# Kernel optimization log

Hardware: AMD Instinct MI355X
Metric: run time of the kernel (lower is better)

The kernel has to match this reference:

```python
import jax, jax.numpy as jnp
import numpy as np

# Dims: B=4, C_in=256, H=W=64 -> L=4096, token_dim D=256, state_dim N=512, K=4
B_, C_IN, H_, W_ = 4, 256, 64, 64
D, N, K = 256, 512, 4


def setup_inputs() -> dict:
    key = jax.random.key(0)
    ks = jax.random.split(key, 16)
    g = lambda k, shape, sc=0.02: (jax.random.normal(k, shape, jnp.float32) * sc)
    return {
        'feat_map': jax.random.normal(ks[0], (B_, C_IN, H_, W_), jnp.float32),
        'hf_map':   jax.random.normal(ks[1], (B_, C_IN, H_, W_), jnp.float32),
        # 1x1 conv proj_f / proj_hf: weight (out=D, in=C_IN), bias (D,)
        'Wf':  g(ks[2], (D, C_IN)), 'bf':  jnp.zeros((D,), jnp.float32),
        'Whf': g(ks[3], (D, C_IN)), 'bhf': jnp.zeros((D,), jnp.float32),
        # alpha_head: Linear(D, D//2) -> GELU -> Linear(D//2, K)
        'Wa1': g(ks[4], (D // 2, D)), 'ba1': jnp.zeros((D // 2,), jnp.float32),
        'Wa2': g(ks[5], (K, D // 2)), 'ba2': jnp.zeros((K,), jnp.float32),
        # SelectiveSSM base tuples: diagonal decay logits A (K,N), input maps B (K,N,D), output maps C (K,D,N)
        'A_base': g(ks[6], (K, N), 1.0),
        'B_base': g(ks[7], (K, N, D), 0.02),
        'C_base': g(ks[8], (K, D, N), 0.02),
        # out_proj 1x1 conv: (C_IN, D)
        'Wout': g(ks[9], (C_IN, D)), 'bout': jnp.zeros((C_IN,), jnp.float32),
    }


def _stage(feat_map, hf_map, Wf, bf, Whf, bhf, Wa1, ba1, Wa2, ba2,
           A_base, B_base, C_base, Wout, bout):
    B, C, H, W = feat_map.shape
    L = H * W
    # 1x1 conv token projections -> (B, L, D)
    t_f = jnp.einsum('bchw,dc->bdhw', feat_map, Wf) + bf[None, :, None, None]
    t_hf = jnp.einsum('bchw,dc->bdhw', hf_map, Whf) + bhf[None, :, None, None]
    x = t_f.reshape(B, -1, L).transpose(0, 2, 1)        # (B, L, D)
    t_hf_seq = t_hf.reshape(B, -1, L).transpose(0, 2, 1)  # (B, L, D)
    # gating MLP -> per-token mixture weights over K base SSMs
    hmid = jax.nn.gelu(t_hf_seq @ Wa1.T + ba1, approximate=False)
    alpha = jax.nn.softmax(hmid @ Wa2.T + ba2, axis=-1)  # (B, L, K)
    # selective SSM: per-token mixed diagonal decay and input drive
    a = jax.nn.sigmoid(jnp.einsum('blk,kn->bln', alpha, A_base))   # (B, L, N)
    u = jnp.einsum('bld,blk,knd->bln', x, alpha, B_base)           # (B, L, N)

    def step(h, au):
        a_t, u_t = au                   # each (B, N)
        h = a_t * h + u_t
        return h, h

    h0 = jnp.zeros((B, a.shape[-1]), x.dtype)
    _, hs = jax.lax.scan(step, h0, (a.transpose(1, 0, 2), u.transpose(1, 0, 2)))
    h_seq = hs.transpose(1, 0, 2)                                   # (B, L, N)
    # mixed readout
    y = jnp.einsum('blk,bln,kdn->bld', alpha, h_seq, C_base)        # (B, L, D)
    y_map = y.transpose(0, 2, 1).reshape(B, -1, H, W)
    out = jnp.einsum('bdhw,cd->bchw', y_map, Wout) + bout[None, :, None, None]
    return out


def reference(feat_map, hf_map, Wf, bf, Whf, bhf, Wa1, ba1, Wa2, ba2,
              A_base, B_base, C_base, Wout, bout):
    return _stage(feat_map, hf_map, Wf, bf, Whf, bhf, Wa1, ba1, Wa2, ba2,
                  A_base, B_base, C_base, Wout, bout)
```

## Files before the change

kernel.cpp:

```cpp
#include <hip/hip_runtime.h>
#include <hip/hip_bf16.h>
#include <math.h>

#define B_  4
#define CIN 256
#define L_  4096
#define D_  256
#define N_  512
#define K_  4
#define DH  128
#define BL  (B_ * L_)

#define NCHUNK 128
#define CLEN   (L_ / NCHUNK)

typedef __attribute__((ext_vector_type(8))) short bfrag;
typedef __attribute__((ext_vector_type(4))) float f4;

__device__ __forceinline__ float bf2f(unsigned short u) {
  return __uint_as_float(((unsigned int)u) << 16);
}
__device__ __forceinline__ unsigned short f2bf(float f) {
  unsigned int u = __float_as_uint(f);
  return (unsigned short)((u + 0x7FFFu + ((u >> 16) & 1u)) >> 16);
}

__global__ void k_prep(const float* __restrict__ Wf, const float* __restrict__ Whf,
                       const float* __restrict__ Wa1, const float* __restrict__ Wout,
                       const float* __restrict__ Bb, const float* __restrict__ Cb,
                       const float* __restrict__ bfv, const float* __restrict__ bhfv,
                       unsigned short* __restrict__ Wfb ,
                       unsigned short* __restrict__ Wa1b,
                       unsigned short* __restrict__ Woutb,
                       unsigned short* __restrict__ Bb16,
                       unsigned short* __restrict__ Cb16,
                       float* __restrict__ biascat) {
  int i = blockIdx.x * 256 + threadIdx.x;
  if (i < 65536) { Wfb[i] = f2bf(Wf[i]); return; } i -= 65536;
  if (i < 65536) { Wfb[65536 + i] = f2bf(Whf[i]); return; } i -= 65536;
  if (i < 32768) { Wa1b[i] = f2bf(Wa1[i]); return; } i -= 32768;
  if (i < 65536) { Woutb[i] = f2bf(Wout[i]); return; } i -= 65536;
  if (i < 524288) {
    int d = i & 255, n = (i >> 8) & 511, k = i >> 17;
    Bb16[(((size_t)n << 2) | k) << 8 | d] = f2bf(Bb[i]);
    return;
  } i -= 524288;
  if (i < 524288) {
    int nn = i & 511, d = (i >> 9) & 255, k = i >> 17;
    Cb16[(((size_t)d << 2) | k) << 9 | nn] = f2bf(Cb[i]);
    return;
  } i -= 524288;
  if (i < 256) { biascat[i] = bfv[i]; return; } i -= 256;
  if (i < 256) { biascat[256 + i] = bhfv[i]; }
}

__global__ void k_transpose2(const float* __restrict__ feat, const float* __restrict__ hf,
                             unsigned short* __restrict__ featT ) {
  __shared__ float tile[32][33];
  const int z = blockIdx.z;
  const int b = z & 3, which = z >> 2;
  const float* in = which ? hf : feat;
  unsigned short* outT = featT + (size_t)which * BL * CIN;
  const int l0 = blockIdx.x * 32, c0 = blockIdx.y * 32;
  const int tx = threadIdx.x, ty = threadIdx.y;
  const float* p = in + ((size_t)b * CIN + c0 + ty) * L_ + l0 + tx;
#pragma unroll
  for (int i = 0; i < 32; i += 8) tile[ty + i][tx] = p[(size_t)i * L_];
  __syncthreads();
  unsigned short* q = outT + ((size_t)b * L_ + l0 + ty) * CIN + c0 + tx;
#pragma unroll
  for (int i = 0; i < 32; i += 8) q[(size_t)i * CIN] = f2bf(tile[tx][ty + i]);
}

__global__ void k_alpha(const unsigned short* __restrict__ hm0,
                        const unsigned short* __restrict__ hm1,
                        const float* __restrict__ ba1, const float* __restrict__ Wa2,
                        const float* __restrict__ ba2, float* __restrict__ alpha) {
  __shared__ float w2[K_ * DH];
  __shared__ float b1[DH];
  __shared__ float b2[K_];
  for (int i = threadIdx.x; i < K_ * DH; i += 256) w2[i] = Wa2[i];
  if (threadIdx.x < DH) b1[threadIdx.x] = ba1[threadIdx.x];
  if (threadIdx.x < K_) b2[threadIdx.x] = ba2[threadIdx.x];
  __syncthreads();
  const int token = blockIdx.x * 64 + (threadIdx.x >> 2);
  const int q = threadIdx.x & 3;
  float a0 = 0.f, a1 = 0.f, a2 = 0.f, a3 = 0.f;
  const size_t base = (size_t)token * DH + q * 32;
#pragma unroll
  for (int j8 = 0; j8 < 4; ++j8) {
    uint4 v0 = *(const uint4*)(hm0 + base + j8 * 8);
    uint4 v1 = *(const uint4*)(hm1 + base + j8 * 8);
    const unsigned int* pa = (const unsigned int*)&v0;
    const unsigned int* pb = (const unsigned int*)&v1;
#pragma unroll
    for (int p = 0; p < 4; ++p) {
      float h0 = bf2f((unsigned short)(pa[p] & 0xffffu)) +
                 bf2f((unsigned short)(pb[p] & 0xffffu));
      float h1 = bf2f((unsigned short)(pa[p] >> 16)) +
                 bf2f((unsigned short)(pb[p] >> 16));
      const int d = q * 32 + j8 * 8 + p * 2;
      float g0 = h0 + b1[d];
      float g1 = h1 + b1[d + 1];
      g0 = 0.5f * g0 * (1.0f + erff(g0 * 0.70710678118654752f));
      g1 = 0.5f * g1 * (1.0f + erff(g1 * 0.70710678118654752f));
      a0 += g0 * w2[0 * DH + d] + g1 * w2[0 * DH + d + 1];
      a1 += g0 * w2[1 * DH + d] + g1 * w2[1 * DH + d + 1];
      a2 += g0 * w2[2 * DH + d] + g1 * w2[2 * DH + d + 1];
      a3 += g0 * w2[3 * DH + d] + g1 * w2[3 * DH + d + 1];
    }
  }
  a0 += __shfl_xor(a0, 1); a1 += __shfl_xor(a1, 1); a2 += __shfl_xor(a2, 1); a3 += __shfl_xor(a3, 1);
  a0 += __shfl_xor(a0, 2); a1 += __shfl_xor(a1, 2); a2 += __shfl_xor(a2, 2); a3 += __shfl_xor(a3, 2);
  a0 += b2[0]; a1 += b2[1]; a2 += b2[2]; a3 += b2[3];
  float m = fmaxf(fmaxf(a0, a1), fmaxf(a2, a3));
  float e0 = expf(a0 - m), e1 = expf(a1 - m), e2 = expf(a2 - m), e3 = expf(a3 - m);
  float inv = 1.f / (e0 + e1 + e2 + e3);
  float my = (q == 0) ? e0 : (q == 1) ? e1 : (q == 2) ? e2 : e3;
  alpha[(size_t)token * 4 + q] = my * inv;
}


__global__ void k_scanA(const unsigned short* __restrict__ u, const float* __restrict__ alpha,
                        const float* __restrict__ Abase,
                        float* __restrict__ P, float* __restrict__ Hend) {
  const int n = threadIdx.x;
  const int bc = blockIdx.x;
  const int b = bc >> 7, c = bc & 127;
  const float A0 = Abase[n], A1 = Abase[N_ + n], A2 = Abase[2 * N_ + n], A3 = Abase[3 * N_ + n];
  const size_t tok0 = (size_t)b * L_ + (size_t)c * CLEN;
  float p = 1.f, h = 0.f;
  for (int l = 0; l < CLEN; ++l) {
    const size_t t = tok0 + l;
    float4 al = *(const float4*)(alpha + t * 4);
    float s = al.x * A0 + al.y * A1 + al.z * A2 + al.w * A3;
    float av = 1.f / (1.f + expf(-s));
    float uv = bf2f(u[t * N_ + n]);
    h = av * h + uv;
    p *= av;
  }
  P[(size_t)bc * N_ + n] = p;
  Hend[(size_t)bc * N_ + n] = h;
}

__global__ void k_scanB(const float* __restrict__ P, const float* __restrict__ Hend,
                        float* __restrict__ Hstart) {
  const int n = threadIdx.x;
  const int b = blockIdx.x;
  float h = 0.f;
  for (int c = 0; c < NCHUNK; ++c) {
    size_t idx = ((size_t)b * NCHUNK + c) * N_ + n;
    Hstart[idx] = h;
    h = P[idx] * h + Hend[idx];
  }
}

__global__ void k_scanC(const unsigned short* __restrict__ u, const float* __restrict__ alpha,
                        const float* __restrict__ Abase, const float* __restrict__ Hstart,
                        unsigned short* __restrict__ hbf) {
  const int n = threadIdx.x;
  const int bc = blockIdx.x;
  const int b = bc >> 7, c = bc & 127;
  const float A0 = Abase[n], A1 = Abase[N_ + n], A2 = Abase[2 * N_ + n], A3 = Abase[3 * N_ + n];
  const size_t tok0 = (size_t)b * L_ + (size_t)c * CLEN;
  float h = Hstart[(size_t)bc * N_ + n];
  for (int l = 0; l < CLEN; ++l) {
    const size_t t = tok0 + l;
    float4 al = *(const float4*)(alpha + t * 4);
    float s = al.x * A0 + al.y * A1 + al.z * A2 + al.w * A3;
    float av = 1.f / (1.f + expf(-s));
    float uv = bf2f(u[t * N_ + n]);
    h = av * h + uv;
    hbf[t * N_ + n] = f2bf(h);
  }
}

#define BM 128
#define BN 128
#define BK 32

#define GLL(src, dst)                                                                      \
  __builtin_amdgcn_global_load_lds((const __attribute__((address_space(1))) void*)(src),   \
                                   (__attribute__((address_space(3))) void*)(dst), 16, 0, 0)

#define BM2 128
#define BN2 256

template <int BIAS, int EPI>
__global__ __launch_bounds__(512, 2) void gemm_bt2(
    const unsigned short* __restrict__ A, long sA,
    const unsigned short* __restrict__ Bm, long sB,
    const float* __restrict__ bias, long bS,
    const float* __restrict__ alphaP,
    void* __restrict__ Cv, long sC,
    int M, int N, int Kd, int lda, int ldb) {
  const int zb = blockIdx.z;
  A += (size_t)zb * sA;
  Bm += (size_t)zb * sB;
  if (BIAS) bias += (size_t)zb * bS;
  const int m0 = blockIdx.x * BM2;
  const int n0 = blockIdx.y * BN2;
  __shared__ __attribute__((aligned(16))) unsigned short As[3 * BM2 * BK];
  __shared__ __attribute__((aligned(16))) unsigned short Bs[3 * BN2 * BK];
  const int t = threadIdx.x;
  const int lane = t & 63;
  const int w = t >> 6;
  const int wm = (w >> 2) * 64;
  const int wn = (w & 3) * 64;

  f4 acc[4][4];
#pragma unroll
  for (int i = 0; i < 4; ++i)
#pragma unroll
    for (int j = 0; j < 4; ++j) acc[i][j] = (f4){0.f, 0.f, 0.f, 0.f};

  const int rS = t >> 2;
  const int cS = (((t & 3) ^ ((t >> 3) & 3))) * 8;
  const unsigned short* gA = A + (size_t)(m0 + rS) * lda + cS;
  const unsigned short* gB = Bm + (size_t)(n0 + rS) * ldb + cS;
  const long rowStepB = (long)128 * ldb;
  const int r16 = lane & 15;
  const int sx = (r16 >> 1) & 3;
  const int kg = (((lane >> 4) ^ sx)) * 8;

#define STAGE2(slot, kt)                                                \
  do {                                                                  \
    const unsigned short* sA_ = gA + (size_t)(kt) * BK;                 \
    const unsigned short* sB_ = gB + (size_t)(kt) * BK;                 \
    unsigned short* dA_ = As + (slot) * (BM2 * BK) + t * 8;             \
    unsigned short* dB_ = Bs + (slot) * (BN2 * BK) + t * 8;             \
    GLL(sA_, dA_);                                                      \
    GLL(sB_, dB_);                                                      \
    GLL(sB_ + rowStepB, dB_ + BM2 * BK);                                \
  } while (0)

  const int nIter = Kd / BK;
  STAGE2(0, 0);
  STAGE2(1, 1);
  int slot = 0;
  for (int kt = 0; kt < nIter; ++kt) {
    if (kt + 1 < nIter) asm volatile("s_waitcnt vmcnt(3)" ::: "memory");
    else                asm volatile("s_waitcnt vmcnt(0)" ::: "memory");
    __builtin_amdgcn_s_barrier();
    asm volatile("" ::: "memory");
    if (kt + 2 < nIter) {
      int s2 = slot + 2; if (s2 >= 3) s2 -= 3;
      STAGE2(s2, kt + 2);
    }
    const unsigned short* Ab = As + slot * (BM2 * BK);
    const unsigned short* Bb2 = Bs + slot * (BN2 * BK);
    bfrag af[4], bfr[4];
#pragma unroll
    for (int i = 0; i < 4; ++i) {
      af[i]  = *(const bfrag*)(Ab + (wm + i * 16 + r16) * BK + kg);
      bfr[i] = *(const bfrag*)(Bb2 + (wn + i * 16 + r16) * BK + kg);
    }
    __builtin_amdgcn_s_setprio(1);
#pragma unroll
    for (int i = 0; i < 4; ++i)
#pragma unroll
      for (int j = 0; j < 4; ++j)
        acc[i][j] = __builtin_amdgcn_mfma_f32_16x16x32_bf16(af[i], bfr[j], acc[i][j], 0, 0, 0);
    __builtin_amdgcn_s_setprio(0);
    asm volatile("" ::: "memory");
    slot = (slot == 2) ? 0 : slot + 1;
  }
#undef STAGE2

  const int rowBase = m0 + wm + ((lane >> 4) << 2);
  const int colBase = n0 + wn + (lane & 15);

  if (EPI >= 2) {
    const int kq = lane & 3;
    const int NO = N >> 2;
    float av[4][4];
#pragma unroll
    for (int i = 0; i < 4; ++i)
#pragma unroll
      for (int r = 0; r < 4; ++r)
        av[i][r] = alphaP[(size_t)(rowBase + i * 16 + r) * 4 + kq];
    float* Cf = (float*)Cv + (size_t)zb * sC;
    unsigned short* Cb = (unsigned short*)Cv + (size_t)zb * sC;
#pragma unroll
    for (int i = 0; i < 4; ++i)
#pragma unroll
      for (int j = 0; j < 4; ++j) {
        const int col = colBase + j * 16;
#pragma unroll
        for (int r = 0; r < 4; ++r) {
          float p = av[i][r] * acc[i][j][r];
          p += __shfl_xor(p, 1);
          p += __shfl_xor(p, 2);
          if (kq == 0) {
            const int row = rowBase + i * 16 + r;
            if (EPI == 2) Cf[(size_t)row * NO + (col >> 2)] = p;
            else          Cb[(size_t)row * NO + (col >> 2)] = f2bf(p);
          }
        }
      }
    return;
  }

  float* Cf = (float*)Cv + (size_t)zb * sC;
  unsigned short* Cb = (unsigned short*)Cv + (size_t)zb * sC;
#pragma unroll
  for (int i = 0; i < 4; ++i) {
#pragma unroll
    for (int j = 0; j < 4; ++j) {
      const int col = colBase + j * 16;
#pragma unroll
      for (int r = 0; r < 4; ++r) {
        const int row = rowBase + i * 16 + r;
        float v = acc[i][j][r];
        if (BIAS == 1) v += bias[col];
        if (BIAS == 2) v += bias[row];
        if (EPI == 1) Cb[(size_t)row * N + col] = f2bf(v);
        else          Cf[(size_t)row * N + col] = v;
      }
    }
  }
}

template <int BIAS, int EPI >
__global__ __launch_bounds__(512, 2) void gemm_w8(
    const unsigned short* __restrict__ A, long sA,
    const unsigned short* __restrict__ Bm, long sB,
    const float* __restrict__ bias, long bS,
    void* __restrict__ Cv, long sC,
    int M, int N, int Kd, int lda, int ldb) {
  const int zb = blockIdx.z;
  A += (size_t)zb * sA;
  Bm += (size_t)zb * sB;
  if (BIAS) bias += (size_t)zb * bS;
  const int m0 = blockIdx.x * BM;
  const int n0 = blockIdx.y * BN;
  __shared__ __attribute__((aligned(16))) unsigned short As[3 * BM * BK];
  __shared__ __attribute__((aligned(16))) unsigned short Bs[3 * BN * BK];
  const int t = threadIdx.x;
  const int lane = t & 63;
  const int w = t >> 6;
  const int wm = (w >> 2) * 64;
  const int wn = (w & 3) * 32;

  f4 acc[4][2];
#pragma unroll
  for (int i = 0; i < 4; ++i)
#pragma unroll
    for (int j = 0; j < 2; ++j) acc[i][j] = (f4){0.f, 0.f, 0.f, 0.f};

  const int rS = t >> 2;
  const int cS = (((t & 3) ^ ((t >> 3) & 3))) * 8;
  const unsigned short* gA = A + (size_t)(m0 + rS) * lda + cS;
  const unsigned short* gB = Bm + (size_t)(n0 + rS) * ldb + cS;
  const int r16 = lane & 15;
  const int sx = (r16 >> 1) & 3;
  const int kg = (((lane >> 4) ^ sx)) * 8;

#define STAGEW(slot, kt)                                                \
  do {                                                                  \
    GLL(gA + (size_t)(kt) * BK, As + (slot) * (BM * BK) + t * 8);       \
    GLL(gB + (size_t)(kt) * BK, Bs + (slot) * (BN * BK) + t * 8);       \
  } while (0)

  const int nIter = Kd / BK;
  STAGEW(0, 0);
  STAGEW(1, 1);
  int slot = 0;
  for (int kt = 0; kt < nIter; ++kt) {
    if (kt + 1 < nIter) asm volatile("s_waitcnt vmcnt(2)" ::: "memory");
    else                asm volatile("s_waitcnt vmcnt(0)" ::: "memory");
    __builtin_amdgcn_s_barrier();
    asm volatile("" ::: "memory");
    if (kt + 2 < nIter) {
      int s2 = slot + 2; if (s2 >= 3) s2 -= 3;
      STAGEW(s2, kt + 2);
    }
    const unsigned short* Ab = As + slot * (BM * BK);
    const unsigned short* Bb2 = Bs + slot * (BN * BK);
    bfrag af[4], bfr[2];
#pragma unroll
    for (int i = 0; i < 4; ++i)
      af[i]  = *(const bfrag*)(Ab + (wm + i * 16 + r16) * BK + kg);
#pragma unroll
    for (int j = 0; j < 2; ++j)
      bfr[j] = *(const bfrag*)(Bb2 + (wn + j * 16 + r16) * BK + kg);
    __builtin_amdgcn_s_setprio(1);
#pragma unroll
    for (int i = 0; i < 4; ++i)
#pragma unroll
      for (int j = 0; j < 2; ++j)
        acc[i][j] = __builtin_amdgcn_mfma_f32_16x16x32_bf16(af[i], bfr[j], acc[i][j], 0, 0, 0);
    __builtin_amdgcn_s_setprio(0);
    asm volatile("" ::: "memory");
    slot = (slot == 2) ? 0 : slot + 1;
  }
#undef STAGEW

  const int rowBase = m0 + wm + ((lane >> 4) << 2);
  const int colBase = n0 + wn + (lane & 15);
  float* Cf = (float*)Cv + (size_t)zb * sC;
  unsigned short* Cb = (unsigned short*)Cv + (size_t)zb * sC;
#pragma unroll
  for (int i = 0; i < 4; ++i) {
#pragma unroll
    for (int j = 0; j < 2; ++j) {
      const int col = colBase + j * 16;
#pragma unroll
      for (int r = 0; r < 4; ++r) {
        const int row = rowBase + i * 16 + r;
        float v = acc[i][j][r];
        if (BIAS == 1) v += bias[col];
        if (BIAS == 2) v += bias[row];
        if (EPI == 1) Cb[(size_t)row * N + col] = f2bf(v);
        else          Cf[(size_t)row * N + col] = v;
      }
    }
  }
}


extern "C" void kernel_launch(void* const* d_in, const int* in_sizes, int n_in,
                              void* d_out, int out_size, void* d_ws, size_t ws_size,
                              hipStream_t stream) {
  const float* feat  = (const float*)d_in[0];
  const float* hf    = (const float*)d_in[1];
  const float* Wf    = (const float*)d_in[2];
  const float* bfv   = (const float*)d_in[3];
  const float* Whf   = (const float*)d_in[4];
  const float* bhfv  = (const float*)d_in[5];
  const float* Wa1   = (const float*)d_in[6];
  const float* ba1   = (const float*)d_in[7];
  const float* Wa2   = (const float*)d_in[8];
  const float* ba2   = (const float*)d_in[9];
  const float* Abase = (const float*)d_in[10];
  const float* Bbase = (const float*)d_in[11];
  const float* Cbase = (const float*)d_in[12];
  const float* Wout  = (const float*)d_in[13];
  const float* bout  = (const float*)d_in[14];
  float* out = (float*)d_out;

  char* ws = (char*)d_ws;
  size_t off = 0;
  auto alloc = [&](size_t bytes) { void* p = ws + off; off += bytes; return p; };

  unsigned short* Wfb    = (unsigned short*)alloc((size_t)2 * D_ * CIN * 2);
  unsigned short* Wa1b   = (unsigned short*)alloc((size_t)DH * D_ * 2);
  unsigned short* Woutb  = (unsigned short*)alloc((size_t)CIN * D_ * 2);
  unsigned short* Bb16   = (unsigned short*)alloc((size_t)K_ * N_ * D_ * 2);
  unsigned short* Cb16   = (unsigned short*)alloc((size_t)K_ * D_ * N_ * 2);
  float*          biascat= (float*)alloc((size_t)2 * D_ * 4);
  float*          alpha  = (float*)alloc((size_t)BL * K_ * 4);
  float*          Pc     = (float*)alloc((size_t)B_ * NCHUNK * N_ * 4);
  float*          He     = (float*)alloc((size_t)B_ * NCHUNK * N_ * 4);
  float*          Hs     = (float*)alloc((size_t)B_ * NCHUNK * N_ * 4);
  unsigned short* hbf    = (unsigned short*)alloc((size_t)BL * N_ * 2);
  unsigned short* x      = (unsigned short*)alloc((size_t)BL * D_ * 2);
  unsigned short* thf    = (unsigned short*)alloc((size_t)BL * D_ * 2);
  unsigned short* featT  = (unsigned short*)alloc((size_t)BL * CIN * 2);
  unsigned short* hfT    = (unsigned short*)alloc((size_t)BL * CIN * 2);
  unsigned short* u16    = (unsigned short*)alloc((size_t)BL * N_ * 2);

  unsigned short* hm0 = featT;
  unsigned short* hm1 = featT + (size_t)BL * DH;
  unsigned short* y   = thf;

  if (ws_size < off) return;

  k_prep<<<dim3((3 * 65536 + 32768 + 2 * 524288 + 512 + 255) / 256), 256, 0, stream>>>(
      Wf, Whf, Wa1, Wout, Bbase, Cbase, bfv, bhfv, Wfb, Wa1b, Woutb, Bb16, Cb16, biascat);

  k_transpose2<<<dim3(L_ / 32, CIN / 32, 2 * B_), dim3(32, 8), 0, stream>>>(feat, hf, featT);

  gemm_w8<1, 1><<<dim3(BL / BM, D_ / BN, 2), 512, 0, stream>>>(
      featT, (long)BL * CIN, Wfb, (long)D_ * CIN, biascat, D_,
      x, (long)BL * D_, BL, D_, CIN, CIN, CIN);

  gemm_w8<0, 1><<<dim3(BL / BM, DH / BN, 2), 512, 0, stream>>>(
      thf, 128, Wa1b, 128, nullptr, 0,
      hm0, (long)BL * DH, BL, DH, 128, D_, D_);
  k_alpha<<<dim3(BL / 64), 256, 0, stream>>>(hm0, hm1, ba1, Wa2, ba2, alpha);

  gemm_bt2<0, 3><<<dim3(BL / BM2, (K_ * N_) / BN2, 1), 512, 0, stream>>>(
      x, 0, Bb16, 0, nullptr, 0, alpha, u16, 0, BL, K_ * N_, D_, D_, D_);

  k_scanA<<<dim3(B_ * NCHUNK), N_, 0, stream>>>(u16, alpha, Abase, Pc, He);
  k_scanB<<<dim3(B_), N_, 0, stream>>>(Pc, He, Hs);
  k_scanC<<<dim3(B_ * NCHUNK), N_, 0, stream>>>(u16, alpha, Abase, Hs, hbf);

  gemm_bt2<0, 3><<<dim3(BL / BM2, (K_ * D_) / BN2, 1), 512, 0, stream>>>(
      hbf, 0, Cb16, 0, nullptr, 0, alpha, y, 0, BL, K_ * D_, N_, N_, N_);

  gemm_w8<2, 0><<<dim3(CIN / BM, L_ / BN, B_), 512, 0, stream>>>(
      Woutb, 0, y, (long)L_ * D_, bout, 0, out, (long)CIN * L_, CIN, L_, D_, D_, D_);
}
```

Baseline: 156.0 us.

## Fold proj_hf into alpha-head weights and use larger 256x256 GEMM tiles

A new kernel precomputes the composed weight Wa1·Whf and bias Wa1·bhf+ba1, so the gating MLP's first layer reads hf tokens directly and the separate hf projection GEMM and its intermediate buffer go away. The bt2 GEMM used for the u and y mixtures is replaced by a 256x256-tile version in which each wave holds 8x4 accumulator fragments, raising data reuse per tile. The composed weight is rounded to bf16, which slightly changes numerics. The larger tile raises register and LDS pressure and produces fewer workgroups, which may reduce occupancy.

New measurement: 188.2 us. 20.6% more time.

```diff
diff --git a/kernel.cpp b/kernel.cpp
--- a/kernel.cpp
+++ b/kernel.cpp
@@ -25,33 +25,44 @@
   return (unsigned short)((u + 0x7FFFu + ((u >> 16) & 1u)) >> 16);
 }
 
-__global__ void k_prep(const float* __restrict__ Wf, const float* __restrict__ Whf,
-                       const float* __restrict__ Wa1, const float* __restrict__ Wout,
+__global__ void k_prep(const float* __restrict__ Wf, const float* __restrict__ Wout,
                        const float* __restrict__ Bb, const float* __restrict__ Cb,
-                       const float* __restrict__ bfv, const float* __restrict__ bhfv,
-                       unsigned short* __restrict__ Wfb ,
-                       unsigned short* __restrict__ Wa1b,
+                       unsigned short* __restrict__ Wfb,
                        unsigned short* __restrict__ Woutb,
                        unsigned short* __restrict__ Bb16,
-                       unsigned short* __restrict__ Cb16,
-                       float* __restrict__ biascat) {
+                       unsigned short* __restrict__ Cb16) {
   int i = blockIdx.x * 256 + threadIdx.x;
   if (i < 65536) { Wfb[i] = f2bf(Wf[i]); return; } i -= 65536;
-  if (i < 65536) { Wfb[65536 + i] = f2bf(Whf[i]); return; } i -= 65536;
-  if (i < 32768) { Wa1b[i] = f2bf(Wa1[i]); return; } i -= 32768;
   if (i < 65536) { Woutb[i] = f2bf(Wout[i]); return; } i -= 65536;
   if (i < 524288) {
     int d = i & 255, n = (i >> 8) & 511, k = i >> 17;
     Bb16[(((size_t)n << 2) | k) << 8 | d] = f2bf(Bb[i]);
     return;
   } i -= 524288;
-  if (i < 524288) {
-    int nn = i & 511, d = (i >> 9) & 255, k = i >> 17;
-    Cb16[(((size_t)d << 2) | k) << 9 | nn] = f2bf(Cb[i]);
-    return;
-  } i -= 524288;
-  if (i < 256) { biascat[i] = bfv[i]; return; } i -= 256;
-  if (i < 256) { biascat[256 + i] = bhfv[i]; }
+  int nn = i & 511, d = (i >> 9) & 255, k = i >> 17;
+  Cb16[(((size_t)d << 2) | k) << 9 | nn] = f2bf(Cb[i]);
+}
+
+__global__ void k_compose(const float* __restrict__ Wa1, const float* __restrict__ Whf,
+                          const float* __restrict__ bhf, const float* __restrict__ ba1,
+                          unsigned short* __restrict__ Wcb, float* __restrict__ bc) {
+  __shared__ float row[CIN];
+  __shared__ float red[CIN];
+  const int j = blockIdx.x;
+  const int c = threadIdx.x;
+  row[c] = Wa1[(size_t)j * CIN + c];
+  __syncthreads();
+  float s = 0.f;
+#pragma unroll 8
+  for (int d = 0; d < CIN; ++d) s += row[d] * Whf[(size_t)d * CIN + c];
+  Wcb[(size_t)j * CIN + c] = f2bf(s);
+  red[c] = row[c] * bhf[c];
+  __syncthreads();
+  for (int st = CIN / 2; st > 0; st >>= 1) {
+    if (c < st) red[c] += red[c + st];
+    __syncthreads();
+  }
+  if (c == 0) bc[j] = red[0] + ba1[j];
 }
 
 __global__ void k_transpose2(const float* __restrict__ feat, const float* __restrict__ hf,
@@ -74,13 +85,13 @@
 
 __global__ void k_alpha(const unsigned short* __restrict__ hm0,
                         const unsigned short* __restrict__ hm1,
-                        const float* __restrict__ ba1, const float* __restrict__ Wa2,
+                        const float* __restrict__ bc, const float* __restrict__ Wa2,
                         const float* __restrict__ ba2, float* __restrict__ alpha) {
   __shared__ float w2[K_ * DH];
   __shared__ float b1[DH];
   __shared__ float b2[K_];
   for (int i = threadIdx.x; i < K_ * DH; i += 256) w2[i] = Wa2[i];
-  if (threadIdx.x < DH) b1[threadIdx.x] = ba1[threadIdx.x];
+  if (threadIdx.x < DH) b1[threadIdx.x] = bc[threadIdx.x];
   if (threadIdx.x < K_) b2[threadIdx.x] = ba2[threadIdx.x];
   __syncthreads();
   const int token = blockIdx.x * 64 + (threadIdx.x >> 2);
@@ -183,81 +194,75 @@
   __builtin_amdgcn_global_load_lds((const __attribute__((address_space(1))) void*)(src),   \
                                    (__attribute__((address_space(3))) void*)(dst), 16, 0, 0)
 
-#define BM2 128
-#define BN2 256
-
-template <int BIAS, int EPI>
-__global__ __launch_bounds__(512, 2) void gemm_bt2(
-    const unsigned short* __restrict__ A, long sA,
-    const unsigned short* __restrict__ Bm, long sB,
-    const float* __restrict__ bias, long bS,
+#define BM5 256
+#define BN5 256
+
+__global__ __launch_bounds__(512, 2) void gemm_fat(
+    const unsigned short* __restrict__ A,
+    const unsigned short* __restrict__ Bm,
     const float* __restrict__ alphaP,
-    void* __restrict__ Cv, long sC,
-    int M, int N, int Kd, int lda, int ldb) {
-  const int zb = blockIdx.z;
-  A += (size_t)zb * sA;
-  Bm += (size_t)zb * sB;
-  if (BIAS) bias += (size_t)zb * bS;
-  const int m0 = blockIdx.x * BM2;
-  const int n0 = blockIdx.y * BN2;
-  __shared__ __attribute__((aligned(16))) unsigned short As[3 * BM2 * BK];
-  __shared__ __attribute__((aligned(16))) unsigned short Bs[3 * BN2 * BK];
+    unsigned short* __restrict__ C,
+    int N, int Kd) {
+  const int m0 = blockIdx.x * BM5;
+  const int n0 = blockIdx.y * BN5;
+  __shared__ __attribute__((aligned(16))) unsigned short As[3 * BM5 * BK];
+  __shared__ __attribute__((aligned(16))) unsigned short Bs[3 * BN5 * BK];
   const int t = threadIdx.x;
   const int lane = t & 63;
   const int w = t >> 6;
-  const int wm = (w >> 2) * 64;
+  const int wm = (w >> 2) * 128;
   const int wn = (w & 3) * 64;
 
-  f4 acc[4][4];
-#pragma unroll
-  for (int i = 0; i < 4; ++i)
+  f4 acc[8][4];
+#pragma unroll
+  for (int i = 0; i < 8; ++i)
 #pragma unroll
     for (int j = 0; j < 4; ++j) acc[i][j] = (f4){0.f, 0.f, 0.f, 0.f};
 
   const int rS = t >> 2;
   const int cS = (((t & 3) ^ ((t >> 3) & 3))) * 8;
-  const unsigned short* gA = A + (size_t)(m0 + rS) * lda + cS;
-  const unsigned short* gB = Bm + (size_t)(n0 + rS) * ldb + cS;
-  const long rowStepB = (long)128 * ldb;
+  const unsigned short* gA = A + (size_t)(m0 + rS) * Kd + cS;
+  const unsigned short* gB = Bm + (size_t)(n0 + rS) * Kd + cS;
+  const long rowStep = (long)128 * Kd;
   const int r16 = lane & 15;
   const int sx = (r16 >> 1) & 3;
   const int kg = (((lane >> 4) ^ sx)) * 8;
 
-#define STAGE2(slot, kt)                                                \
+#define STAGE5(slot, kt)                                                \
   do {                                                                  \
     const unsigned short* sA_ = gA + (size_t)(kt) * BK;                 \
     const unsigned short* sB_ = gB + (size_t)(kt) * BK;                 \
-    unsigned short* dA_ = As + (slot) * (BM2 * BK) + t * 8;             \
-    unsigned short* dB_ = Bs + (slot) * (BN2 * BK) + t * 8;             \
-    GLL(sA_, dA_);                                                      \
-    GLL(sB_, dB_);                                                      \
-    GLL(sB_ + rowStepB, dB_ + BM2 * BK);                                \
+    unsigned short* dA_ = As + (slot) * (BM5 * BK) + t * 8;             \
+    unsigned short* dB_ = Bs + (slot) * (BN5 * BK) + t * 8;             \
+    GLL(sA_, dA_); GLL(sA_ + rowStep, dA_ + 128 * BK);                  \
+    GLL(sB_, dB_); GLL(sB_ + rowStep, dB_ + 128 * BK);                  \
   } while (0)
 
   const int nIter = Kd / BK;
-  STAGE2(0, 0);
-  STAGE2(1, 1);
+  STAGE5(0, 0);
+  STAGE5(1, 1);
   int slot = 0;
   for (int kt = 0; kt < nIter; ++kt) {
-    if (kt + 1 < nIter) asm volatile("s_waitcnt vmcnt(3)" ::: "memory");
+    if (kt + 1 < nIter) asm volatile("s_waitcnt vmcnt(4)" ::: "memory");
     else                asm volatile("s_waitcnt vmcnt(0)" ::: "memory");
     __builtin_amdgcn_s_barrier();
     asm volatile("" ::: "memory");
     if (kt + 2 < nIter) {
       int s2 = slot + 2; if (s2 >= 3) s2 -= 3;
-      STAGE2(s2, kt + 2);
+      STAGE5(s2, kt + 2);
     }
-    const unsigned short* Ab = As + slot * (BM2 * BK);
-    const unsigned short* Bb2 = Bs + slot * (BN2 * BK);
-    bfrag af[4], bfr[4];
-#pragma unroll
-    for (int i = 0; i < 4; ++i) {
+    const unsigned short* Ab = As + slot * (BM5 * BK);
+    const unsigned short* Bb2 = Bs + slot * (BN5 * BK);
+    bfrag af[8], bfr[4];
+#pragma unroll
+    for (int i = 0; i < 8; ++i)
       af[i]  = *(const bfrag*)(Ab + (wm + i * 16 + r16) * BK + kg);
-      bfr[i] = *(const bfrag*)(Bb2 + (wn + i * 16 + r16) * BK + kg);
-    }
+#pragma unroll
+    for (int j = 0; j < 4; ++j)
+      bfr[j] = *(const bfrag*)(Bb2 + (wn + j * 16 + r16) * BK + kg);
     __builtin_amdgcn_s_setprio(1);
 #pragma unroll
-    for (int i = 0; i < 4; ++i)
+    for (int i = 0; i < 8; ++i)
 #pragma unroll
       for (int j = 0; j < 4; ++j)
         acc[i][j] = __builtin_amdgcn_mfma_f32_16x16x32_bf16(af[i], bfr[j], acc[i][j], 0, 0, 0);
@@ -265,60 +270,31 @@
     asm volatile("" ::: "memory");
     slot = (slot == 2) ? 0 : slot + 1;
   }
-#undef STAGE2
+#undef STAGE5
 
   const int rowBase = m0 + wm + ((lane >> 4) << 2);
-  const int colBase = n0 + wn + (lane & 15);
-
-  if (EPI >= 2) {
-    const int kq = lane & 3;
-    const int NO = N >> 2;
-    float av[4][4];
-#pragma unroll
-    for (int i = 0; i < 4; ++i)
-#pragma unroll
-      for (int r = 0; r < 4; ++r)
-        av[i][r] = alphaP[(size_t)(rowBase + i * 16 + r) * 4 + kq];
-    float* Cf = (float*)Cv + (size_t)zb * sC;
-    unsigned short* Cb = (unsigned short*)Cv + (size_t)zb * sC;
-#pragma unroll
-    for (int i = 0; i < 4; ++i)
-#pragma unroll
-      for (int j = 0; j < 4; ++j) {
-        const int col = colBase + j * 16;
-#pragma unroll
-        for (int r = 0; r < 4; ++r) {
-          float p = av[i][r] * acc[i][j][r];
-          p += __shfl_xor(p, 1);
-          p += __shfl_xor(p, 2);
-          if (kq == 0) {
-            const int row = rowBase + i * 16 + r;
-            if (EPI == 2) Cf[(size_t)row * NO + (col >> 2)] = p;
-            else          Cb[(size_t)row * NO + (col >> 2)] = f2bf(p);
-          }
-        }
-      }
-    return;
-  }
-
-  float* Cf = (float*)Cv + (size_t)zb * sC;
-  unsigned short* Cb = (unsigned short*)Cv + (size_t)zb * sC;
-#pragma unroll
-  for (int i = 0; i < 4; ++i) {
+  const int colBase = n0 + wn + r16;
+  const int kq = lane & 3;
+  const int NO = N >> 2;
+  float av[8][4];
+#pragma unroll
+  for (int i = 0; i < 8; ++i)
+#pragma unroll
+    for (int r = 0; r < 4; ++r)
+      av[i][r] = alphaP[(size_t)(rowBase + i * 16 + r) * 4 + kq];
+#pragma unroll
+  for (int i = 0; i < 8; ++i)
 #pragma unroll
     for (int j = 0; j < 4; ++j) {
       const int col = colBase + j * 16;
 #pragma unroll
       for (int r = 0; r < 4; ++r) {
-        const int row = rowBase + i * 16 + r;
-        float v = acc[i][j][r];
-        if (BIAS == 1) v += bias[col];
-        if (BIAS == 2) v += bias[row];
-        if (EPI == 1) Cb[(size_t)row * N + col] = f2bf(v);
-        else          Cf[(size_t)row * N + col] = v;
+        float p = av[i][r] * acc[i][j][r];
+        p += __shfl_xor(p, 1);
+        p += __shfl_xor(p, 2);
+        if (kq == 0) C[(size_t)(rowBase + i * 16 + r) * NO + (col >> 2)] = f2bf(p);
       }
     }
-  }
 }
 
 template <int BIAS, int EPI >
@@ -443,52 +419,52 @@
   size_t off = 0;
   auto alloc = [&](size_t bytes) { void* p = ws + off; off += bytes; return p; };
 
-  unsigned short* Wfb    = (unsigned short*)alloc((size_t)2 * D_ * CIN * 2);
-  unsigned short* Wa1b   = (unsigned short*)alloc((size_t)DH * D_ * 2);
+  unsigned short* Wfb    = (unsigned short*)alloc((size_t)D_ * CIN * 2);
   unsigned short* Woutb  = (unsigned short*)alloc((size_t)CIN * D_ * 2);
+  unsigned short* Wcb    = (unsigned short*)alloc((size_t)DH * CIN * 2);
+  float*          bc     = (float*)alloc((size_t)DH * 4);
   unsigned short* Bb16   = (unsigned short*)alloc((size_t)K_ * N_ * D_ * 2);
   unsigned short* Cb16   = (unsigned short*)alloc((size_t)K_ * D_ * N_ * 2);
-  float*          biascat= (float*)alloc((size_t)2 * D_ * 4);
   float*          alpha  = (float*)alloc((size_t)BL * K_ * 4);
   float*          Pc     = (float*)alloc((size_t)B_ * NCHUNK * N_ * 4);
   float*          He     = (float*)alloc((size_t)B_ * NCHUNK * N_ * 4);
   float*          Hs     = (float*)alloc((size_t)B_ * NCHUNK * N_ * 4);
   unsigned short* hbf    = (unsigned short*)alloc((size_t)BL * N_ * 2);
   unsigned short* x      = (unsigned short*)alloc((size_t)BL * D_ * 2);
-  unsigned short* thf    = (unsigned short*)alloc((size_t)BL * D_ * 2);
   unsigned short* featT  = (unsigned short*)alloc((size_t)BL * CIN * 2);
   unsigned short* hfT    = (unsigned short*)alloc((size_t)BL * CIN * 2);
   unsigned short* u16    = (unsigned short*)alloc((size_t)BL * N_ * 2);
 
   unsigned short* hm0 = featT;
   unsigned short* hm1 = featT + (size_t)BL * DH;
-  unsigned short* y   = thf;
+  unsigned short* y   = x;
 
   if (ws_size < off) return;
 
-  k_prep<<<dim3((3 * 65536 + 32768 + 2 * 524288 + 512 + 255) / 256), 256, 0, stream>>>(
-      Wf, Whf, Wa1, Wout, Bbase, Cbase, bfv, bhfv, Wfb, Wa1b, Woutb, Bb16, Cb16, biascat);
+  k_prep<<<dim3((2 * 65536 + 2 * 524288) / 256), 256, 0, stream>>>(
+      Wf, Wout, Bbase, Cbase, Wfb, Woutb, Bb16, Cb16);
+  k_compose<<<dim3(DH), CIN, 0, stream>>>(Wa1, Whf, bhfv, ba1, Wcb, bc);
 
   k_transpose2<<<dim3(L_ / 32, CIN / 32, 2 * B_), dim3(32, 8), 0, stream>>>(feat, hf, featT);
 
-  gemm_w8<1, 1><<<dim3(BL / BM, D_ / BN, 2), 512, 0, stream>>>(
-      featT, (long)BL * CIN, Wfb, (long)D_ * CIN, biascat, D_,
-      x, (long)BL * D_, BL, D_, CIN, CIN, CIN);
+  gemm_w8<1, 1><<<dim3(BL / BM, D_ / BN, 1), 512, 0, stream>>>(
+      featT, 0, Wfb, 0, bfv, 0,
+      x, 0, BL, D_, CIN, CIN, CIN);
 
   gemm_w8<0, 1><<<dim3(BL / BM, DH / BN, 2), 512, 0, stream>>>(
-      thf, 128, Wa1b, 128, nullptr, 0,
-      hm0, (long)BL * DH, BL, DH, 128, D_, D_);
-  k_alpha<<<dim3(BL / 64), 256, 0, stream>>>(hm0, hm1, ba1, Wa2, ba2, alpha);
-
-  gemm_bt2<0, 3><<<dim3(BL / BM2, (K_ * N_) / BN2, 1), 512, 0, stream>>>(
-      x, 0, Bb16, 0, nullptr, 0, alpha, u16, 0, BL, K_ * N_, D_, D_, D_);
+      hfT, 128, Wcb, 128, nullptr, 0,
+      hm0, (long)BL * DH, BL, DH, 128, CIN, CIN);
+  k_alpha<<<dim3(BL / 64), 256, 0, stream>>>(hm0, hm1, bc, Wa2, ba2, alpha);
+
+  gemm_fat<<<dim3(BL / BM5, (K_ * N_) / BN5), 512, 0, stream>>>(
+      x, Bb16, alpha, u16, K_ * N_, D_);
 
   k_scanA<<<dim3(B_ * NCHUNK), N_, 0, stream>>>(u16, alpha, Abase, Pc, He);
   k_scanB<<<dim3(B_), N_, 0, stream>>>(Pc, He, Hs);
   k_scanC<<<dim3(B_ * NCHUNK), N_, 0, stream>>>(u16, alpha, Abase, Hs, hbf);
 
-  gemm_bt2<0, 3><<<dim3(BL / BM2, (K_ * D_) / BN2, 1), 512, 0, stream>>>(
-      hbf, 0, Cb16, 0, nullptr, 0, alpha, y, 0, BL, K_ * D_, N_, N_, N_);
+  gemm_fat<<<dim3(BL / BM5, (K_ * D_) / BN5), 512, 0, stream>>>(
+      hbf, Cb16, alpha, y, K_ * D_, N_);
 
   gemm_w8<2, 0><<<dim3(CIN / BM, L_ / BN, B_), 512, 0, stream>>>(
       Woutb, 0, y, (long)L_ * D_, bout, 0, out, (long)CIN * L_, CIN, L_, D_, D_, D_);
```

## Fold hf projection into gating MLP weights and vectorize scan kernels

Applied to the files above, without the earlier changes.

Precomputes the composed weight Wa1·Whf and bias on device, so the gating GEMM reads the transposed hf input directly and the t_hf projection GEMM is dropped. The first projection GEMM now computes only x. The three scan kernels each handle two state channels per thread with paired loads and stores, halving thread count. This adds a small compose kernel and changes bf16 rounding points in the gating path.

Result: slower. 171.9 us (+10.2%).

```diff
diff --git a/kernel.cpp b/kernel.cpp
--- a/kernel.cpp
+++ b/kernel.cpp
@@ -25,33 +25,44 @@
   return (unsigned short)((u + 0x7FFFu + ((u >> 16) & 1u)) >> 16);
 }
 
-__global__ void k_prep(const float* __restrict__ Wf, const float* __restrict__ Whf,
-                       const float* __restrict__ Wa1, const float* __restrict__ Wout,
+__global__ void k_prep(const float* __restrict__ Wf, const float* __restrict__ Wout,
                        const float* __restrict__ Bb, const float* __restrict__ Cb,
-                       const float* __restrict__ bfv, const float* __restrict__ bhfv,
-                       unsigned short* __restrict__ Wfb ,
-                       unsigned short* __restrict__ Wa1b,
+                       unsigned short* __restrict__ Wfb,
                        unsigned short* __restrict__ Woutb,
                        unsigned short* __restrict__ Bb16,
-                       unsigned short* __restrict__ Cb16,
-                       float* __restrict__ biascat) {
+                       unsigned short* __restrict__ Cb16) {
   int i = blockIdx.x * 256 + threadIdx.x;
   if (i < 65536) { Wfb[i] = f2bf(Wf[i]); return; } i -= 65536;
-  if (i < 65536) { Wfb[65536 + i] = f2bf(Whf[i]); return; } i -= 65536;
-  if (i < 32768) { Wa1b[i] = f2bf(Wa1[i]); return; } i -= 32768;
   if (i < 65536) { Woutb[i] = f2bf(Wout[i]); return; } i -= 65536;
   if (i < 524288) {
     int d = i & 255, n = (i >> 8) & 511, k = i >> 17;
     Bb16[(((size_t)n << 2) | k) << 8 | d] = f2bf(Bb[i]);
     return;
   } i -= 524288;
-  if (i < 524288) {
-    int nn = i & 511, d = (i >> 9) & 255, k = i >> 17;
-    Cb16[(((size_t)d << 2) | k) << 9 | nn] = f2bf(Cb[i]);
-    return;
-  } i -= 524288;
-  if (i < 256) { biascat[i] = bfv[i]; return; } i -= 256;
-  if (i < 256) { biascat[256 + i] = bhfv[i]; }
+  int nn = i & 511, d = (i >> 9) & 255, k = i >> 17;
+  Cb16[(((size_t)d << 2) | k) << 9 | nn] = f2bf(Cb[i]);
+}
+
+__global__ void k_compose(const float* __restrict__ Wa1, const float* __restrict__ Whf,
+                          const float* __restrict__ bhf, const float* __restrict__ ba1,
+                          unsigned short* __restrict__ Wcb, float* __restrict__ bc) {
+  __shared__ float row[CIN];
+  __shared__ float red[CIN];
+  const int j = blockIdx.x;
+  const int c = threadIdx.x;
+  row[c] = Wa1[(size_t)j * CIN + c];
+  __syncthreads();
+  float s = 0.f;
+#pragma unroll 8
+  for (int d = 0; d < CIN; ++d) s += row[d] * Whf[(size_t)d * CIN + c];
+  Wcb[(size_t)j * CIN + c] = f2bf(s);
+  red[c] = row[c] * bhf[c];
+  __syncthreads();
+  for (int st = CIN / 2; st > 0; st >>= 1) {
+    if (c < st) red[c] += red[c + st];
+    __syncthreads();
+  }
+  if (c == 0) bc[j] = red[0] + ba1[j];
 }
 
 __global__ void k_transpose2(const float* __restrict__ feat, const float* __restrict__ hf,
@@ -74,13 +85,13 @@
 
 __global__ void k_alpha(const unsigned short* __restrict__ hm0,
                         const unsigned short* __restrict__ hm1,
-                        const float* __restrict__ ba1, const float* __restrict__ Wa2,
+                        const float* __restrict__ bc, const float* __restrict__ Wa2,
                         const float* __restrict__ ba2, float* __restrict__ alpha) {
   __shared__ float w2[K_ * DH];
   __shared__ float b1[DH];
   __shared__ float b2[K_];
   for (int i = threadIdx.x; i < K_ * DH; i += 256) w2[i] = Wa2[i];
-  if (threadIdx.x < DH) b1[threadIdx.x] = ba1[threadIdx.x];
+  if (threadIdx.x < DH) b1[threadIdx.x] = bc[threadIdx.x];
   if (threadIdx.x < K_) b2[threadIdx.x] = ba2[threadIdx.x];
   __syncthreads();
   const int token = blockIdx.x * 64 + (threadIdx.x >> 2);
@@ -124,54 +135,71 @@
 __global__ void k_scanA(const unsigned short* __restrict__ u, const float* __restrict__ alpha,
                         const float* __restrict__ Abase,
                         float* __restrict__ P, float* __restrict__ Hend) {
-  const int n = threadIdx.x;
+  const int n = threadIdx.x * 2;
   const int bc = blockIdx.x;
   const int b = bc >> 7, c = bc & 127;
-  const float A0 = Abase[n], A1 = Abase[N_ + n], A2 = Abase[2 * N_ + n], A3 = Abase[3 * N_ + n];
+  const float2 A0 = *(const float2*)(Abase + n);
+  const float2 A1 = *(const float2*)(Abase + N_ + n);
+  const float2 A2 = *(const float2*)(Abase + 2 * N_ + n);
+  const float2 A3 = *(const float2*)(Abase + 3 * N_ + n);
   const size_t tok0 = (size_t)b * L_ + (size_t)c * CLEN;
-  float p = 1.f, h = 0.f;
+  float p0 = 1.f, h0 = 0.f, p1 = 1.f, h1 = 0.f;
   for (int l = 0; l < CLEN; ++l) {
     const size_t t = tok0 + l;
     float4 al = *(const float4*)(alpha + t * 4);
-    float s = al.x * A0 + al.y * A1 + al.z * A2 + al.w * A3;
-    float av = 1.f / (1.f + expf(-s));
-    float uv = bf2f(u[t * N_ + n]);
-    h = av * h + uv;
-    p *= av;
-  }
-  P[(size_t)bc * N_ + n] = p;
-  Hend[(size_t)bc * N_ + n] = h;
+    float s0 = al.x * A0.x + al.y * A1.x + al.z * A2.x + al.w * A3.x;
+    float s1 = al.x * A0.y + al.y * A1.y + al.z * A2.y + al.w * A3.y;
+    float av0 = 1.f / (1.f + expf(-s0));
+    float av1 = 1.f / (1.f + expf(-s1));
+    unsigned int uv = *(const unsigned int*)(u + t * N_ + n);
+    h0 = av0 * h0 + bf2f((unsigned short)(uv & 0xffffu));
+    h1 = av1 * h1 + bf2f((unsigned short)(uv >> 16));
+    p0 *= av0; p1 *= av1;
+  }
+  *(float2*)(P + (size_t)bc * N_ + n) = (float2){p0, p1};
+  *(float2*)(Hend + (size_t)bc * N_ + n) = (float2){h0, h1};
 }
 
 __global__ void k_scanB(const float* __restrict__ P, const float* __restrict__ Hend,
                         float* __restrict__ Hstart) {
-  const int n = threadIdx.x;
+  const int n = threadIdx.x * 2;
   const int b = blockIdx.x;
-  float h = 0.f;
+  float h0 = 0.f, h1 = 0.f;
   for (int c = 0; c < NCHUNK; ++c) {
     size_t idx = ((size_t)b * NCHUNK + c) * N_ + n;
-    Hstart[idx] = h;
-    h = P[idx] * h + Hend[idx];
+    *(float2*)(Hstart + idx) = (float2){h0, h1};
+    float2 p = *(const float2*)(P + idx);
+    float2 he = *(const float2*)(Hend + idx);
+    h0 = p.x * h0 + he.x;
+    h1 = p.y * h1 + he.y;
   }
 }
 
 __global__ void k_scanC(const unsigned short* __restrict__ u, const float* __restrict__ alpha,
                         const float* __restrict__ Abase, const float* __restrict__ Hstart,
                         unsigned short* __restrict__ hbf) {
-  const int n = threadIdx.x;
+  const int n = threadIdx.x * 2;
   const int bc = blockIdx.x;
   const int b = bc >> 7, c = bc & 127;
-  const float A0 = Abase[n], A1 = Abase[N_ + n], A2 = Abase[2 * N_ + n], A3 = Abase[3 * N_ + n];
+  const float2 A0 = *(const float2*)(Abase + n);
+  const float2 A1 = *(const float2*)(Abase + N_ + n);
+  const float2 A2 = *(const float2*)(Abase + 2 * N_ + n);
+  const float2 A3 = *(const float2*)(Abase + 3 * N_ + n);
   const size_t tok0 = (size_t)b * L_ + (size_t)c * CLEN;
-  float h = Hstart[(size_t)bc * N_ + n];
+  float2 hs = *(const float2*)(Hstart + (size_t)bc * N_ + n);
+  float h0 = hs.x, h1 = hs.y;
   for (int l = 0; l < CLEN; ++l) {
     const size_t t = tok0 + l;
     float4 al = *(const float4*)(alpha + t * 4);
-    float s = al.x * A0 + al.y * A1 + al.z * A2 + al.w * A3;
-    float av = 1.f / (1.f + expf(-s));
-    float uv = bf2f(u[t * N_ + n]);
-    h = av * h + uv;
-    hbf[t * N_ + n] = f2bf(h);
+    float s0 = al.x * A0.x + al.y * A1.x + al.z * A2.x + al.w * A3.x;
+    float s1 = al.x * A0.y + al.y * A1.y + al.z * A2.y + al.w * A3.y;
+    float av0 = 1.f / (1.f + expf(-s0));
+    float av1 = 1.f / (1.f + expf(-s1));
+    unsigned int uv = *(const unsigned int*)(u + t * N_ + n);
+    h0 = av0 * h0 + bf2f((unsigned short)(uv & 0xffffu));
+    h1 = av1 * h1 + bf2f((unsigned short)(uv >> 16));
+    *(unsigned int*)(hbf + t * N_ + n) =
+        (unsigned int)f2bf(h0) | ((unsigned int)f2bf(h1) << 16);
   }
 }
 
@@ -443,49 +471,49 @@
   size_t off = 0;
   auto alloc = [&](size_t bytes) { void* p = ws + off; off += bytes; return p; };
 
-  unsigned short* Wfb    = (unsigned short*)alloc((size_t)2 * D_ * CIN * 2);
-  unsigned short* Wa1b   = (unsigned short*)alloc((size_t)DH * D_ * 2);
+  unsigned short* Wfb    = (unsigned short*)alloc((size_t)D_ * CIN * 2);
   unsigned short* Woutb  = (unsigned short*)alloc((size_t)CIN * D_ * 2);
+  unsigned short* Wcb    = (unsigned short*)alloc((size_t)DH * CIN * 2);
+  float*          bc     = (float*)alloc((size_t)DH * 4);
   unsigned short* Bb16   = (unsigned short*)alloc((size_t)K_ * N_ * D_ * 2);
   unsigned short* Cb16   = (unsigned short*)alloc((size_t)K_ * D_ * N_ * 2);
-  float*          biascat= (float*)alloc((size_t)2 * D_ * 4);
   float*          alpha  = (float*)alloc((size_t)BL * K_ * 4);
   float*          Pc     = (float*)alloc((size_t)B_ * NCHUNK * N_ * 4);
   float*          He     = (float*)alloc((size_t)B_ * NCHUNK * N_ * 4);
   float*          Hs     = (float*)alloc((size_t)B_ * NCHUNK * N_ * 4);
   unsigned short* hbf    = (unsigned short*)alloc((size_t)BL * N_ * 2);
   unsigned short* x      = (unsigned short*)alloc((size_t)BL * D_ * 2);
-  unsigned short* thf    = (unsigned short*)alloc((size_t)BL * D_ * 2);
   unsigned short* featT  = (unsigned short*)alloc((size_t)BL * CIN * 2);
   unsigned short* hfT    = (unsigned short*)alloc((size_t)BL * CIN * 2);
   unsigned short* u16    = (unsigned short*)alloc((size_t)BL * N_ * 2);
 
   unsigned short* hm0 = featT;
   unsigned short* hm1 = featT + (size_t)BL * DH;
-  unsigned short* y   = thf;
+  unsigned short* y   = x;
 
   if (ws_size < off) return;
 
-  k_prep<<<dim3((3 * 65536 + 32768 + 2 * 524288 + 512 + 255) / 256), 256, 0, stream>>>(
-      Wf, Whf, Wa1, Wout, Bbase, Cbase, bfv, bhfv, Wfb, Wa1b, Woutb, Bb16, Cb16, biascat);
+  k_prep<<<dim3((2 * 65536 + 2 * 524288) / 256), 256, 0, stream>>>(
+      Wf, Wout, Bbase, Cbase, Wfb, Woutb, Bb16, Cb16);
+  k_compose<<<dim3(DH), CIN, 0, stream>>>(Wa1, Whf, bhfv, ba1, Wcb, bc);
 
   k_transpose2<<<dim3(L_ / 32, CIN / 32, 2 * B_), dim3(32, 8), 0, stream>>>(feat, hf, featT);
 
-  gemm_w8<1, 1><<<dim3(BL / BM, D_ / BN, 2), 512, 0, stream>>>(
-      featT, (long)BL * CIN, Wfb, (long)D_ * CIN, biascat, D_,
-      x, (long)BL * D_, BL, D_, CIN, CIN, CIN);
+  gemm_w8<1, 1><<<dim3(BL / BM, D_ / BN, 1), 512, 0, stream>>>(
+      featT, 0, Wfb, 0, bfv, 0,
+      x, 0, BL, D_, CIN, CIN, CIN);
 
   gemm_w8<0, 1><<<dim3(BL / BM, DH / BN, 2), 512, 0, stream>>>(
-      thf, 128, Wa1b, 128, nullptr, 0,
-      hm0, (long)BL * DH, BL, DH, 128, D_, D_);
-  k_alpha<<<dim3(BL / 64), 256, 0, stream>>>(hm0, hm1, ba1, Wa2, ba2, alpha);
+      hfT, 128, Wcb, 128, nullptr, 0,
+      hm0, (long)BL * DH, BL, DH, 128, CIN, CIN);
+  k_alpha<<<dim3(BL / 64), 256, 0, stream>>>(hm0, hm1, bc, Wa2, ba2, alpha);
 
   gemm_bt2<0, 3><<<dim3(BL / BM2, (K_ * N_) / BN2, 1), 512, 0, stream>>>(
       x, 0, Bb16, 0, nullptr, 0, alpha, u16, 0, BL, K_ * N_, D_, D_, D_);
 
-  k_scanA<<<dim3(B_ * NCHUNK), N_, 0, stream>>>(u16, alpha, Abase, Pc, He);
-  k_scanB<<<dim3(B_), N_, 0, stream>>>(Pc, He, Hs);
-  k_scanC<<<dim3(B_ * NCHUNK), N_, 0, stream>>>(u16, alpha, Abase, Hs, hbf);
+  k_scanA<<<dim3(B_ * NCHUNK), N_ / 2, 0, stream>>>(u16, alpha, Abase, Pc, He);
+  k_scanB<<<dim3(B_), N_ / 2, 0, stream>>>(Pc, He, Hs);
+  k_scanC<<<dim3(B_ * NCHUNK), N_ / 2, 0, stream>>>(u16, alpha, Abase, Hs, hbf);
 
   gemm_bt2<0, 3><<<dim3(BL / BM2, (K_ * D_) / BN2, 1), 512, 0, stream>>>(
       hbf, 0, Cb16, 0, nullptr, 0, alpha, y, 0, BL, K_ * D_, N_, N_, N_);
```
